# Optimization experiments

Hardware: AMD Instinct MI355X
Metric: run time of the kernel (lower is better)

The kernel has to match this reference:

```python
import jax, jax.numpy as jnp
import numpy as np

B, NQ, NK, D, H = 4, 1025, 1024, 1024, 16
C = D // H          # per-head channels = 64
DFF = 1024          # FFN hidden, hard-coded in source
LN_EPS = 1e-5


def setup_inputs() -> dict:
    key = jax.random.key(0)
    ks = jax.random.split(key, 12)
    s = 0.02
    return {
        "q": jax.random.normal(ks[0], (B, NQ, D), jnp.float32),
        "k": jax.random.normal(ks[1], (B, NK, D), jnp.float32),
        "v": jax.random.normal(ks[2], (B, NK, D), jnp.float32),
        "w_qk": jax.random.normal(ks[3], (D, D), jnp.float32) * s,
        "dummy": jax.random.normal(ks[4], (1, D), jnp.float32),
        "w1": jax.random.normal(ks[5], (C, C // 2), jnp.float32) * s,
        "b1": jnp.zeros((C // 2,), jnp.float32),
        "w2": jax.random.normal(ks[6], (C, C // 2), jnp.float32) * s,
        "b2": jnp.zeros((C // 2,), jnp.float32),
        "w3": jax.random.normal(ks[7], (2 * C, C), jnp.float32) * s,
        "b3": jnp.zeros((C,), jnp.float32),
        "fw1": jax.random.normal(ks[8], (C, DFF), jnp.float32) * s,
        "fb1": jnp.zeros((DFF,), jnp.float32),
        "fw2": jax.random.normal(ks[9], (DFF, C), jnp.float32) * s,
        "fb2": jnp.zeros((C,), jnp.float32),
        "ln_g": jnp.ones((C,), jnp.float32),
        "ln_b": jnp.zeros((C,), jnp.float32),
    }


def _split_heads(x):
    # 'b n (h c) -> (b h) n c'
    b, n, _ = x.shape
    return x.reshape(b, n, H, C).transpose(0, 2, 1, 3).reshape(b * H, n, C)


def _l2norm(x):
    n = jnp.linalg.norm(x, axis=-1, keepdims=True)
    return x / jnp.maximum(n, 1e-12)


def reference(q, k, v, w_qk, dummy, w1, b1, w2, b2, w3, b3,
              fw1, fb1, fw2, fb2, ln_g, ln_b):
    b, nq, d = q.shape
    residual = q
    qp = q @ w_qk
    kp = jnp.concatenate(
        [k @ w_qk, jnp.broadcast_to(dummy[None], (b, 1, d))], axis=1)
    vp = jnp.concatenate([v, jnp.zeros((b, 1, d), v.dtype)], axis=1)

    qh, kh, vh, rh = map(_split_heads, (qp, kp, vp, residual))

    # cosine-similarity attention, ReLU instead of softmax (dropout p=0)
    attn = jnp.einsum('bic,bjc->bij', _l2norm(qh), _l2norm(kh))
    attn = jax.nn.relu(attn)
    out = jnp.einsum('bij,bjc->bic', attn, vh)  # (b*h, nq, c)

    o1 = jax.nn.relu((out * rh) @ w1 + b1)
    o2 = jax.nn.relu((rh - out) @ w2 + b2)
    o = jnp.concatenate([o1, o2, rh], axis=-1) @ w3 + b3

    # FFN with residual + LayerNorm (dropouts are identity at p=0)
    t = o + rh
    t = t + (jax.nn.relu(t @ fw1 + fb1) @ fw2 + fb2)
    mu = jnp.mean(t, axis=-1, keepdims=True)
    var = jnp.mean(jnp.square(t - mu), axis=-1, keepdims=True)
    t = (t - mu) / jnp.sqrt(var + LN_EPS) * ln_g + ln_b

    t = t + vh  # requires nq == nk + 1

    # '(b h) n c -> b n (h c)'
    return t.reshape(b, H, nq, C).transpose(0, 2, 1, 3).reshape(b, nq, d)
```

## Files before the change

### kernel.cpp

```cpp
#include <hip/hip_runtime.h>
#include <hip/hip_bf16.h>

#define DEV __device__ __forceinline__

typedef __attribute__((ext_vector_type(4))) float  f32x4;
typedef __attribute__((ext_vector_type(8))) short  s16x8;
typedef __attribute__((ext_vector_type(8))) __bf16 bf16x8;

#define NQ   1025
#define BH   64
#define NPAD 1152
#define MT   65600
#define DFF  1024

DEV short f2bf(float f){
  unsigned u = __builtin_bit_cast(unsigned, f);
  u = u + 0x7fffu + ((u >> 16) & 1u);
  return (short)(u >> 16);
}
DEV float bf2f(short s){
  unsigned u = ((unsigned)(unsigned short)s) << 16;
  return __builtin_bit_cast(float, u);
}
DEV f32x4 zero4(){ f32x4 z; z[0]=0.f; z[1]=0.f; z[2]=0.f; z[3]=0.f; return z; }
DEV s16x8 zero8(){ s16x8 z; for(int e=0;e<8;e++) z[e]=0; return z; }

DEV f32x4 mfma16(s16x8 a, s16x8 b, f32x4 c){
  return __builtin_amdgcn_mfma_f32_16x16x32_bf16(
      __builtin_bit_cast(bf16x8, a), __builtin_bit_cast(bf16x8, b), c, 0, 0, 0);
}

DEV void gll16(const void* g, void* l){
  __builtin_amdgcn_global_load_lds((const __attribute__((address_space(1))) void*)g,
                                   (__attribute__((address_space(3))) void*)l, 16, 0, 0);
}

DEV s16x8 lds_frag(const char* base, int row, int k8){
  int byte = row*128 + k8*2; byte ^= (row & 7) << 4;
  return *(const s16x8*)(base + byte);
}
DEV void lds_write16(char* base, int row, int k8, s16x8 v){
  int byte = row*128 + k8*2; byte ^= (row & 7) << 4;
  *(s16x8*)(base + byte) = v;
}
DEV void lds_write2(char* base, int row, int col, short v){
  int byte = row*128 + col*2; byte ^= (row & 7) << 4;
  *(short*)(base + byte) = v;
}
DEV void lds_w16_256(char* base, int row, int col, s16x8 v){
  int byte = row*256 + col*2; byte ^= (row & 7) << 4;
  *(s16x8*)(base + byte) = v;
}
DEV s16x8 lds_r16_256(const char* base, int row, int col){
  int byte = row*256 + col*2; byte ^= (row & 7) << 4;
  return *(const s16x8*)(base + byte);
}
DEV void lds_w2_256(char* base, int row, int col, short v){
  int byte = row*256 + col*2; byte ^= (row & 7) << 4;
  *(short*)(base + byte) = v;
}
DEV void blob_w16(char* blob, int row, int k8, s16x8 v){
  int byte = row*128 + k8*2; byte ^= (row & 7) << 4;
  *(s16x8*)(blob + byte) = v;
}

__global__ __launch_bounds__(256)
void k_prep(const float* __restrict__ q, const float* __restrict__ kk,
            const float* __restrict__ v, const float* __restrict__ w_qk,
            const float* __restrict__ fw1, const float* __restrict__ fw2,
            char* __restrict__ ab, char* __restrict__ wb,
            char* __restrict__ vb, char* __restrict__ f1B, char* __restrict__ f2B){
  __shared__ float SMF[64*129];
  int bid = blockIdx.x;
  int tid = threadIdx.x;
  if (bid < 1152){
    int mt = bid>>4, kt = bid&15;
    int r = tid>>1, ks = (tid&1)*32;
    int pr = mt*128 + r;
    int part = pr >= 4608;
    int pp = part ? pr-4608 : pr;
    int b = pp/NPAD, i = pp%NPAD;
    const float* src = nullptr;
    if (!part && i < 1025) src = q  + ((long)(b*1025+i))*1024 + kt*64 + ks;
    if ( part && i < 1024) src = kk + ((long)(b*1024+i))*1024 + kt*64 + ks;
    char* blob = ab + ((long)(mt*16+kt))*16384;
    #pragma unroll
    for (int c8=0;c8<32;c8+=8){
      s16x8 vv = zero8();
      if (src){
        f32x4 f0 = *(const f32x4*)(src + c8);
        f32x4 f1 = *(const f32x4*)(src + c8 + 4);
        #pragma unroll
        for(int e=0;e<4;e++){ vv[e]=f2bf(f0[e]); vv[4+e]=f2bf(f1[e]); }
      }
      blob_w16(blob, r, ks+c8, vv);
    }
  } else if (bid < 1280){
    int loc = bid - 1152;
    int nt = loc>>4, kt = loc&15;
    float (*T)[129] = (float(*)[129])SMF;
    for (int idx=tid; idx<8192; idx+=256){
      int kr = idx>>7, nc = idx&127;
      T[kr][nc] = w_qk[(long)(kt*64+kr)*1024 + nt*128+nc];
    }
    __syncthreads();
    int r = tid>>1, ks=(tid&1)*32;
    char* blob = wb + ((long)(nt*16+kt))*16384;
    #pragma unroll
    for (int c8=0;c8<32;c8+=8){
      s16x8 vv;
      #pragma unroll
      for(int e=0;e<8;e++) vv[e] = f2bf(T[ks+c8+e][r]);
      blob_w16(blob, r, ks+c8, vv);
    }
  } else if (bid < 2304){
    int loc = bid - 1280;
    int jt = loc&15, bh = loc>>4;
    int b = bh>>4, h = bh&15;
    float (*T)[65] = (float(*)[65])SMF;
    for (int idx=tid; idx<4096; idx+=256){
      int jr = idx>>6, cc = idx&63;
      int j = jt*64+jr;
      T[jr][cc] = (j<1024)? v[((long)(b*1024+j))*1024 + h*64+cc] : 0.f;
    }
    __syncthreads();
    int r = tid>>2, js=(tid&3)*16;
    char* blob = vb + ((long)(bh*18+jt))*8192;
    #pragma unroll
    for (int c8=0;c8<16;c8+=8){
      s16x8 vv;
      #pragma unroll
      for(int e=0;e<8;e++) vv[e] = f2bf(T[js+c8+e][r]);
      blob_w16(blob, r, js+c8, vv);
    }
  } else {
    int loc = bid - 2304;
    int d = loc&15, which = loc>>4;
    float (*T)[65] = (float(*)[65])SMF;
    for (int idx=tid; idx<4096; idx+=256){
      int r = idx>>6, c = idx&63;
      T[r][c] = (which==0) ? fw1[(long)r*DFF + d*64 + c]
                           : fw2[(long)(d*64+r)*64 + c];
    }
    __syncthreads();
    char* blob = (which==0 ? f1B : f2B) + (long)d*8192;
    int rr = tid>>2, js = (tid&3)*16;
    #pragma unroll
    for (int c8=0;c8<16;c8+=8){
      s16x8 vv;
      #pragma unroll
      for(int e=0;e<8;e++) vv[e] = f2bf(T[js+c8+e][rr]);
      blob_w16(blob, rr, js+c8, vv);
    }
  }
}

__global__ __launch_bounds__(256,2)
void k_proj(const char* __restrict__ ab, const char* __restrict__ wb,
            char* __restrict__ qpB, char* __restrict__ kpB,
            float* __restrict__ qnorm, float* __restrict__ knorm){
  __shared__ char SM[32768];
  char* A = SM; char* Bm = SM+16384;
  int flat = blockIdx.x;
  int g = (flat&7)*72 + (flat>>3);
  int mt = g>>3, nt = g&7;
  int tid=threadIdx.x, lane=tid&63, wv=tid>>6, lr=lane&15, lg=lane>>4;
  f32x4 acc[4][4];
  for(int a=0;a<4;a++) for(int b=0;b<4;b++) acc[a][b]=zero4();
  int wm=(wv>>1)*64, wn=(wv&1)*64;
  for (int kt=0; kt<16; kt++){
    const char* asrc = ab + ((long)(mt*16+kt))*16384 + wv*4096 + lane*16;
    const char* bsrc = wb + ((long)(nt*16+kt))*16384 + wv*4096 + lane*16;
    char* adst = A + wv*4096;  char* bdst = Bm + wv*4096;
    #pragma unroll
    for (int t=0;t<4;t++){
      gll16(asrc + t*1024, adst + t*1024);
      gll16(bsrc + t*1024, bdst + t*1024);
    }
    __syncthreads();
    #pragma unroll
    for (int kc=0;kc<64;kc+=32){
      int lk = kc + (lg<<3);
      s16x8 af[4], bfr[4];
      #pragma unroll
      for(int i=0;i<4;i++) af[i]  = lds_frag(A,  wm + i*16 + lr, lk);
      #pragma unroll
      for(int i=0;i<4;i++) bfr[i] = lds_frag(Bm, wn + i*16 + lr, lk);
      #pragma unroll
      for(int mi=0;mi<4;mi++)
        #pragma unroll
        for(int ni=0;ni<4;ni++) acc[mi][ni] = mfma16(af[mi], bfr[ni], acc[mi][ni]);
    }
    __syncthreads();
  }
  int head = nt*2 + (wv&1);
  #pragma unroll
  for(int mi=0;mi<4;mi++)
  #pragma unroll
  for(int j=0;j<4;j++){
    float ss = 0.f;
    #pragma unroll
    for(int ni=0;ni<4;ni++){ float x=acc[mi][ni][j]; ss += x*x; }
    ss += __shfl_xor(ss,1); ss += __shfl_xor(ss,2);
    ss += __shfl_xor(ss,4); ss += __shfl_xor(ss,8);
    if (lr==0){
      int pr = mt*128 + wm + mi*16 + lg*4 + j;
      int part = pr>=4608; int pp = part? pr-4608:pr;
      int b = pp/NPAD, i = pp%NPAD;
      float scv = 1.f/fmaxf(sqrtf(ss), 1e-12f);
      (part? knorm : qnorm)[(b*16+head)*NPAD + i] = scv;
    }
  }
  #pragma unroll
  for(int mi=0;mi<4;mi++)
  #pragma unroll
  for(int ni=0;ni<4;ni++)
  #pragma unroll
  for(int j=0;j<4;j++)
    lds_w2_256(SM, wm+mi*16+lg*4+j, wn+ni*16+lr, f2bf(acc[mi][ni][j]));
  __syncthreads();
  {
    int r = tid>>1, half = tid&1;
    int pr = mt*128 + r;
    int part = pr>=4608; int pp = part? pr-4608:pr;
    int b = pp/NPAD, i = pp%NPAD;
    int h2 = nt*2 + half;
    char* dst = (part? kpB : qpB) + ((long)((b*16+h2)*18 + (i>>6)))*8192;
    int rr = i&63;
    #pragma unroll
    for (int c8=0;c8<64;c8+=8){
      s16x8 vv = lds_r16_256(SM, r, half*64 + c8);
      blob_w16(dst, rr, c8, vv);
    }
  }
}

__global__ __launch_bounds__(256,2)
void k_attn(const char* __restrict__ qpB, const char* __restrict__ kpB,
            const char* __restrict__ vtB,
            const float* __restrict__ qnorm, const float* __restrict__ knorm,
            short* __restrict__ att){
  __shared__ char SM[49152];
  char* Q = SM; char* KT = SM+16384; char* VT = KT+8192; char* P = VT+8192;
  int flat = blockIdx.x;
  int g = (flat&7)*72 + (flat>>3);
  int bh = g/9, it = g%9;
  int i0 = it*128;
  int tid=threadIdx.x, lane=tid&63, wv=tid>>6, lr=lane&15, lg=lane>>4;
  {
    const char* src = qpB + ((long)(bh*18 + it*2))*8192 + wv*4096 + lane*16;
    char* dst = Q + wv*4096;
    #pragma unroll
    for (int t=0;t<4;t++) gll16(src + t*1024, dst + t*1024);
  }
  float rq[2][4];
  #pragma unroll
  for(int mi=0;mi<2;mi++)
  #pragma unroll
  for(int j=0;j<4;j++)
    rq[mi][j] = qnorm[bh*NPAD + i0 + wv*32+mi*16+lg*4+j];
  f32x4 oacc[2][4];
  for(int a=0;a<2;a++) for(int b=0;b<4;b++) oacc[a][b]=zero4();
  for (int jt=0; jt<16; ++jt){
    {
      const char* ks = kpB + ((long)(bh*18+jt))*8192 + wv*2048 + lane*16;
      const char* vs = vtB + ((long)(bh*18+jt))*8192 + wv*2048 + lane*16;
      gll16(ks,      KT + wv*2048);
      gll16(ks+1024, KT + wv*2048 + 1024);
      gll16(vs,      VT + wv*2048);
      gll16(vs+1024, VT + wv*2048 + 1024);
    }
    float rk[4];
    #pragma unroll
    for(int ni=0;ni<4;ni++) rk[ni] = knorm[bh*NPAD + jt*64 + ni*16+lr];
    __syncthreads();
    f32x4 sc[2][4];
    for(int a=0;a<2;a++) for(int b=0;b<4;b++) sc[a][b]=zero4();
    #pragma unroll
    for(int kc=0;kc<64;kc+=32){
      int lk = kc + (lg<<3);
      s16x8 af[2], bfr[4];
      #pragma unroll
      for(int i=0;i<2;i++) af[i]=lds_frag(Q, wv*32 + i*16 + lr, lk);
      #pragma unroll
      for(int i=0;i<4;i++) bfr[i]=lds_frag(KT, i*16 + lr, lk);
      #pragma unroll
      for(int mi=0;mi<2;mi++)
        #pragma unroll
        for(int ni=0;ni<4;ni++) sc[mi][ni]=mfma16(af[mi],bfr[ni],sc[mi][ni]);
    }
    #pragma unroll
    for(int mi=0;mi<2;mi++)
    #pragma unroll
    for(int ni=0;ni<4;ni++)
    #pragma unroll
    for(int j=0;j<4;j++){
      float x = sc[mi][ni][j] * rq[mi][j] * rk[ni];
      x = x>0.f?x:0.f;
      lds_write2(P, wv*32 + mi*16 + lg*4 + j, ni*16 + lr, f2bf(x));
    }
    __syncthreads();
    #pragma unroll
    for(int kc=0;kc<64;kc+=32){
      int lk = kc + (lg<<3);
      s16x8 pf[2], vf[4];
      #pragma unroll
      for(int i=0;i<2;i++) pf[i]=lds_frag(P, wv*32 + i*16 + lr, lk);
      #pragma unroll
      for(int i=0;i<4;i++) vf[i]=lds_frag(VT, i*16 + lr, lk);
      #pragma unroll
      for(int mi=0;mi<2;mi++)
        #pragma unroll
        for(int ni=0;ni<4;ni++) oacc[mi][ni]=mfma16(pf[mi],vf[ni],oacc[mi][ni]);
    }
    __syncthreads();
  }
  char* OS = SM+16384;
  #pragma unroll
  for(int mi=0;mi<2;mi++)
  #pragma unroll
  for(int ni=0;ni<4;ni++)
  #pragma unroll
  for(int j=0;j<4;j++)
    lds_write2(OS, wv*32+mi*16+lg*4+j, ni*16+lr, f2bf(oacc[mi][ni][j]));
  __syncthreads();
  {
    int r = tid>>1, half = tid&1;
    int i = i0 + r;
    if (i < 1025){
      short* dst = att + ((long)bh*1025 + i)*64 + half*32;
      #pragma unroll
      for (int u=0; u<32; u+=8){
        s16x8 vv = lds_frag(OS, r, half*32 + u);
        *(s16x8*)(dst + u) = vv;
      }
    }
  }
}

__global__ __launch_bounds__(512,4)
void k_tailpre(const short* __restrict__ att, const float* __restrict__ q,
    const float* __restrict__ w1, const float* __restrict__ b1,
    const float* __restrict__ w2, const float* __restrict__ b2,
    const float* __restrict__ w3, const float* __restrict__ b3,
    float* __restrict__ tf){
  __shared__ char SM[73728];
  char* R1 = SM;
  char* R2 = SM + 16384;
  char* R3 = SM + 32768;
  char* WA = SM + 49152;
  char* WB = SM + 53248;
  char* W3 = SM + 57344;
  long m0 = (long)blockIdx.x*128;
  int tid=threadIdx.x, lane=tid&63, wv=tid>>6, lr=lane&15, lg=lane>>4;
  int wr0 = wv*16;
  for (int idx=tid; idx<2048; idx+=512){
    int n=idx>>6, c=idx&63;
    lds_write2(WA, n, c, f2bf(w1[c*32+n]));
    lds_write2(WB, n, c, f2bf(w2[c*32+n]));
  }
  for (int idx=tid; idx<8192; idx+=512){
    int n=idx>>7, kx=idx&127;
    lds_w2_256(W3, n, kx, f2bf(w3[kx*64+n]));
  }
  {
    int r = tid>>2, ks=(tid&3)*16;
    long m = m0 + r;
    if (m < MT){
      int bh=(int)(m/1025); int i=(int)(m-(long)bh*1025); int b=bh>>4, h=bh&15;
      const short* asrc = att + m*64 + ks;
      const float* qsrc = q + ((long)b*1025+i)*1024 + h*64 + ks;
      #pragma unroll
      for (int c8=0;c8<16;c8+=8){
        s16x8 av = *(const s16x8*)(asrc + c8);
        f32x4 q0 = *(const f32x4*)(qsrc + c8);
        f32x4 q1 = *(const f32x4*)(qsrc + c8 + 4);
        s16x8 x1v,x2v,rhv;
        #pragma unroll
        for(int e=0;e<4;e++){
          float o0=bf2f(av[e]),   r0=q0[e];
          float o1=bf2f(av[4+e]), r1=q1[e];
          x1v[e]=f2bf(o0*r0);   x1v[4+e]=f2bf(o1*r1);
          x2v[e]=f2bf(r0-o0);   x2v[4+e]=f2bf(r1-o1);
          rhv[e]=f2bf(r0);      rhv[4+e]=f2bf(r1);
        }
        lds_write16(R1, r, ks+c8, x1v);
        lds_write16(R2, r, ks+c8, x2v);
        lds_write16(R3, r, ks+c8, rhv);
      }
    } else {
      s16x8 z = zero8();
      #pragma unroll
      for (int c8=0;c8<16;c8+=8){
        lds_write16(R1, r, ks+c8, z);
        lds_write16(R2, r, ks+c8, z);
        lds_write16(R3, r, ks+c8, z);
      }
    }
  }
  __syncthreads();
  f32x4 a1[4];
  #pragma unroll
  for(int ni=0;ni<4;ni++) a1[ni]=zero4();
  #pragma unroll
  for (int kc=0;kc<64;kc+=32){
    int lk = kc + (lg<<3);
    s16x8 af1 = lds_frag(R1, wr0+lr, lk);
    s16x8 af2 = lds_frag(R2, wr0+lr, lk);
    s16x8 bw1[2], bw2[2];
    #pragma unroll
    for(int i=0;i<2;i++){
      bw1[i]=lds_frag(WA, i*16+lr, lk);
      bw2[i]=lds_frag(WB, i*16+lr, lk);
    }
    #pragma unroll
    for(int ni=0;ni<2;ni++){
      a1[ni]   = mfma16(af1, bw1[ni], a1[ni]);
      a1[2+ni] = mfma16(af2, bw2[ni], a1[2+ni]);
    }
  }
  float bias12[4];
  #pragma unroll
  for(int ni=0;ni<4;ni++){ int cc=ni*16+lr; bias12[ni] = (cc<32)? b1[cc] : b2[cc-32]; }
  #pragma unroll
  for(int ni=0;ni<4;ni++)
  #pragma unroll
  for(int j=0;j<4;j++){
    float x = a1[ni][j] + bias12[ni];
    x = x>0.f?x:0.f;
    lds_write2(R1, wr0+lg*4+j, ni*16+lr, f2bf(x));
  }
  f32x4 a2[4];
  #pragma unroll
  for(int ni=0;ni<4;ni++) a2[ni]=zero4();
  #pragma unroll
  for (int kc=0;kc<64;kc+=32){
    int lk = kc + (lg<<3);
    s16x8 ao = lds_frag(R1, wr0+lr, lk);
    s16x8 ar = lds_frag(R3, wr0+lr, lk);
    s16x8 bo[4], br[4];
    #pragma unroll
    for(int i=0;i<4;i++){
      bo[i]=lds_r16_256(W3, i*16+lr, lk);
      br[i]=lds_r16_256(W3, i*16+lr, 64+lk);
    }
    #pragma unroll
    for(int ni=0;ni<4;ni++){
      a2[ni]=mfma16(ao, bo[ni], a2[ni]);
      a2[ni]=mfma16(ar, br[ni], a2[ni]);
    }
  }
  float b3v[4];
  #pragma unroll
  for(int ni=0;ni<4;ni++) b3v[ni] = b3[ni*16+lr];
  #pragma unroll
  for(int j=0;j<4;j++){
    long m = m0 + wr0 + lg*4 + j;
    if (m < MT){
      int bh=(int)(m/1025); int i=(int)(m-(long)bh*1025); int b=bh>>4, h=bh&15;
      const float* qsrc = q + ((long)b*1025+i)*1024 + h*64;
      #pragma unroll
      for(int ni=0;ni<4;ni++){
        int cc = ni*16+lr;
        tf[m*64+cc] = a2[ni][j] + b3v[ni] + qsrc[cc];
      }
    }
  }
}

__global__ __launch_bounds__(256,3)
void k_ffn(const float* __restrict__ tf,
      const char* __restrict__ f1B, const char* __restrict__ f2B,
      const float* __restrict__ fb1, const float* __restrict__ fb2,
      const float* __restrict__ ln_g, const float* __restrict__ ln_b,
      const float* __restrict__ v, float* __restrict__ out){
  __shared__ char SM[49152];
  char* T  = SM;
  char* U  = SM + 16384;
  char* W1 = SM + 32768;
  char* W2 = SM + 40960;
  long m0 = (long)blockIdx.x*128;
  int tid=threadIdx.x, lane=tid&63, wv=tid>>6, lr=lane&15, lg=lane>>4;
  {
    int r=tid>>1, ks=(tid&1)*32; long m=m0+r;
    #pragma unroll
    for(int c8=0;c8<32;c8+=8){
      s16x8 vv = zero8();
      if (m<MT){
        f32x4 f0 = *(const f32x4*)(tf + m*64 + ks + c8);
        f32x4 f1 = *(const f32x4*)(tf + m*64 + ks + c8 + 4);
        #pragma unroll
        for(int e=0;e<4;e++){ vv[e]=f2bf(f0[e]); vv[4+e]=f2bf(f1[e]); }
      }
      lds_write16(T, r, ks+c8, vv);
    }
  }
  f32x4 acc2[2][4];
  for(int a=0;a<2;a++) for(int b=0;b<4;b++) acc2[a][b]=zero4();
  for (int d=0; d<16; ++d){
    {
      const char* s1 = f1B + (long)d*8192 + wv*2048 + lane*16;
      const char* s2 = f2B + (long)d*8192 + wv*2048 + lane*16;
      gll16(s1,        W1 + wv*2048);
      gll16(s1 + 1024, W1 + wv*2048 + 1024);
      gll16(s2,        W2 + wv*2048);
      gll16(s2 + 1024, W2 + wv*2048 + 1024);
    }
    __syncthreads();
    f32x4 sc[2][4];
    for(int a=0;a<2;a++) for(int b=0;b<4;b++) sc[a][b]=zero4();
    #pragma unroll
    for(int kc=0;kc<64;kc+=32){
      int lk = kc + (lg<<3);
      s16x8 af[2], bfr[4];
      #pragma unroll
      for(int i=0;i<2;i++) af[i]=lds_frag(T, wv*32+i*16+lr, lk);
      #pragma unroll
      for(int i=0;i<4;i++) bfr[i]=lds_frag(W1, i*16+lr, lk);
      #pragma unroll
      for(int mi=0;mi<2;mi++)
        #pragma unroll
        for(int ni=0;ni<4;ni++) sc[mi][ni]=mfma16(af[mi],bfr[ni],sc[mi][ni]);
    }
    #pragma unroll
    for(int mi=0;mi<2;mi++)
    #pragma unroll
    for(int ni=0;ni<4;ni++)
    #pragma unroll
    for(int j=0;j<4;j++){
      int uc = ni*16+lr;
      float x = sc[mi][ni][j] + fb1[d*64+uc];
      x = x>0.f?x:0.f;
      lds_write2(U, wv*32+mi*16+lg*4+j, uc, f2bf(x));
    }
    #pragma unroll
    for(int kc=0;kc<64;kc+=32){
      int lk = kc + (lg<<3);
      s16x8 uf[2], wf[4];
      #pragma unroll
      for(int i=0;i<2;i++) uf[i]=lds_frag(U, wv*32+i*16+lr, lk);
      #pragma unroll
      for(int i=0;i<4;i++) wf[i]=lds_frag(W2, i*16+lr, lk);
      #pragma unroll
      for(int mi=0;mi<2;mi++)
        #pragma unroll
        for(int ni=0;ni<4;ni++) acc2[mi][ni]=mfma16(uf[mi],wf[ni],acc2[mi][ni]);
    }
    __syncthreads();
  }
  #pragma unroll
  for(int mi=0;mi<2;mi++){
    float xv[4][4];
    long mbase = m0 + wv*32 + mi*16 + lg*4;
    #pragma unroll
    for(int ni=0;ni<4;ni++)
    #pragma unroll
    for(int j=0;j<4;j++){
      long m = mbase + j;
      int c = ni*16+lr;
      float t = (m<MT)? tf[m*64+c] : 0.f;
      xv[ni][j] = acc2[mi][ni][j] + fb2[c] + t;
    }
    #pragma unroll
    for(int j=0;j<4;j++){
      float s = xv[0][j]+xv[1][j]+xv[2][j]+xv[3][j];
      #pragma unroll
      for(int mm=1;mm<16;mm<<=1) s += __shfl_xor(s, mm);
      float mu = s*(1.f/64.f);
      float vs = 0.f;
      #pragma unroll
      for(int ni=0;ni<4;ni++){ float d2=xv[ni][j]-mu; vs += d2*d2; }
      #pragma unroll
      for(int mm=1;mm<16;mm<<=1) vs += __shfl_xor(vs, mm);
      float inv = rsqrtf(vs*(1.f/64.f) + 1e-5f);
      long m = mbase + j;
      if (m < MT){
        int bh = (int)(m/1025); int i = (int)(m - (long)bh*1025);
        int b = bh>>4, h = bh&15;
        #pragma unroll
        for(int ni=0;ni<4;ni++){
          int c = ni*16+lr;
          float y = (xv[ni][j]-mu)*inv*ln_g[c] + ln_b[c];
          float vh = (i<1024)? v[((long)b*1024 + i)*1024 + h*64 + c] : 0.f;
          out[((long)b*1025 + i)*1024 + h*64 + c] = y + vh;
        }
      }
    }
  }
}

extern "C" void kernel_launch(void* const* d_in, const int* in_sizes, int n_in,
                              void* d_out, int out_size, void* d_ws, size_t ws_size,
                              hipStream_t stream) {
  const float* q    = (const float*)d_in[0];
  const float* k    = (const float*)d_in[1];
  const float* v    = (const float*)d_in[2];
  const float* w_qk = (const float*)d_in[3];
  const float* w1   = (const float*)d_in[5];
  const float* b1   = (const float*)d_in[6];
  const float* w2   = (const float*)d_in[7];
  const float* b2   = (const float*)d_in[8];
  const float* w3   = (const float*)d_in[9];
  const float* b3   = (const float*)d_in[10];
  const float* fw1  = (const float*)d_in[11];
  const float* fb1  = (const float*)d_in[12];
  const float* fw2  = (const float*)d_in[13];
  const float* fb2  = (const float*)d_in[14];
  const float* ln_g = (const float*)d_in[15];
  const float* ln_b = (const float*)d_in[16];
  float* out = (float*)d_out;

  char* ws = (char*)d_ws;
  const size_t OFF_A   = 0;
  const size_t SZ_A    = 25190400;
  const size_t OFF_WB  = OFF_A + SZ_A;
  const size_t OFF_F1B = OFF_WB  + (size_t)8*16*16384;
  const size_t OFF_F2B = OFF_F1B + (size_t)16*8192;
  const size_t OFF_VT  = OFF_F2B + (size_t)16*8192;
  const size_t OFF_QP  = OFF_VT  + (size_t)64*18*8192;
  const size_t OFF_KP  = OFF_QP  + (size_t)64*18*8192;
  const size_t OFF_QN  = OFF_KP  + (size_t)64*18*8192;
  const size_t OFF_KN  = OFF_QN  + (size_t)BH*NPAD*4;
  const size_t NEEDED  = OFF_KN  + (size_t)BH*NPAD*4;
  if (ws_size < NEEDED) return;

  char*  ab   = ws + OFF_A;
  short* att  = (short*)(ws + OFF_A);
  float* tf   = (float*)(ws + OFF_A + 8396800);
  char*  wb   = ws + OFF_WB;
  char*  f1B  = ws + OFF_F1B;
  char*  f2B  = ws + OFF_F2B;
  char*  vtB  = ws + OFF_VT;
  char*  qpB  = ws + OFF_QP;
  char*  kpB  = ws + OFF_KP;
  float* qnorm= (float*)(ws + OFF_QN);
  float* knorm= (float*)(ws + OFF_KN);

  k_prep<<<2336, 256, 0, stream>>>(q, k, v, w_qk, fw1, fw2, ab, wb, vtB, f1B, f2B);
  k_proj<<<576, 256, 0, stream>>>(ab, wb, qpB, kpB, qnorm, knorm);
  k_attn<<<576, 256, 0, stream>>>(qpB, kpB, vtB, qnorm, knorm, att);
  k_tailpre<<<513, 512, 0, stream>>>(att, q, w1, b1, w2, b2, w3, b3, tf);
  k_ffn<<<513, 256, 0, stream>>>(tf, f1B, f2B, fb1, fb2, ln_g, ln_b, v, out);
}
```

Before: 179.6 us.

## Handle lone trailing query row separately and skip padded tiles in projection

Query length is 1025, so the last 128-row attention tile held only one real row. That tile is replaced by 64 small blocks, one per batch-head, which compute the final query row with scalar dot products against K and a direct fp32 reduction over V. The projection grid is also cut from 576 to 544 blocks by remapping M-tile indices so that all-padding tiles are skipped. The intent is to remove wasted MFMA work on padding. The cost is a slower scalar path for the tail row, whose strided V reads may lengthen the critical path.

Result: no change. 181.0 us (+0.7%).

```diff
diff --git a/kernel.cpp b/kernel.cpp
--- a/kernel.cpp
+++ b/kernel.cpp
@@ -162,8 +162,9 @@
   __shared__ char SM[32768];
   char* A = SM; char* Bm = SM+16384;
   int flat = blockIdx.x;
-  int g = (flat&7)*72 + (flat>>3);
-  int mt = g>>3, nt = g&7;
+  int g = (flat&7)*68 + (flat>>3);
+  int mtIdx = g>>3, nt = g&7;
+  int mt = (mtIdx < 44) ? mtIdx : (mtIdx + 1 + (mtIdx-44)/8);
   int tid=threadIdx.x, lane=tid&63, wv=tid>>6, lr=lane&15, lg=lane>>4;
   f32x4 acc[4][4];
   for(int a=0;a<4;a++) for(int b=0;b<4;b++) acc[a][b]=zero4();
@@ -239,14 +240,57 @@
 void k_attn(const char* __restrict__ qpB, const char* __restrict__ kpB,
             const char* __restrict__ vtB,
             const float* __restrict__ qnorm, const float* __restrict__ knorm,
-            short* __restrict__ att){
+            const float* __restrict__ v, short* __restrict__ att){
   __shared__ char SM[49152];
+  int flat = blockIdx.x;
+  int tid=threadIdx.x, lane=tid&63, wv=tid>>6, lr=lane&15, lg=lane>>4;
+  if (flat >= 512){
+    int bh = flat - 512;
+    int b = bh>>4, h = bh&15;
+    float* XS = (float*)SM;
+    float* RS = (float*)(SM + 4096);
+    const short* qrow = (const short*)(qpB + ((long)(bh*18+16))*8192);
+    float rqv = qnorm[bh*NPAD + 1024];
+    float qv[64];
+    #pragma unroll
+    for (int c8=0;c8<64;c8+=8){
+      s16x8 qq = *(const s16x8*)(qrow + c8);
+      #pragma unroll
+      for(int e=0;e<8;e++) qv[c8+e] = bf2f(qq[e]);
+    }
+    for (int p=0;p<4;p++){
+      int j = tid + 256*p;
+      const char* kb = kpB + ((long)(bh*18+(j>>6)))*8192;
+      int r = j&63;
+      float S = 0.f;
+      #pragma unroll
+      for (int c8=0;c8<64;c8+=8){
+        s16x8 kv = lds_frag(kb, r, c8);
+        #pragma unroll
+        for(int e=0;e<8;e++) S += qv[c8+e]*bf2f(kv[e]);
+      }
+      float x = S * rqv * knorm[bh*NPAD + j];
+      XS[j] = x>0.f ? x : 0.f;
+    }
+    __syncthreads();
+    float acc = 0.f;
+    const float* vb = v + (long)b*1024*1024 + h*64 + lane;
+    for (int p=0;p<256;p++){
+      int j = wv*256 + p;
+      acc += XS[j] * vb[(long)j*1024];
+    }
+    RS[wv*64 + lane] = acc;
+    __syncthreads();
+    if (tid < 64){
+      float tot = RS[tid] + RS[64+tid] + RS[128+tid] + RS[192+tid];
+      att[((long)bh*1025 + 1024)*64 + tid] = f2bf(tot);
+    }
+    return;
+  }
   char* Q = SM; char* KT = SM+16384; char* VT = KT+8192; char* P = VT+8192;
-  int flat = blockIdx.x;
-  int g = (flat&7)*72 + (flat>>3);
-  int bh = g/9, it = g%9;
+  int g = (flat&7)*64 + (flat>>3);
+  int bh = g>>3, it = g&7;
   int i0 = it*128;
-  int tid=threadIdx.x, lane=tid&63, wv=tid>>6, lr=lane&15, lg=lane>>4;
   {
     const char* src = qpB + ((long)(bh*18 + it*2))*8192 + wv*4096 + lane*16;
     char* dst = Q + wv*4096;
@@ -327,13 +371,11 @@
   {
     int r = tid>>1, half = tid&1;
     int i = i0 + r;
-    if (i < 1025){
-      short* dst = att + ((long)bh*1025 + i)*64 + half*32;
-      #pragma unroll
-      for (int u=0; u<32; u+=8){
-        s16x8 vv = lds_frag(OS, r, half*32 + u);
-        *(s16x8*)(dst + u) = vv;
-      }
+    short* dst = att + ((long)bh*1025 + i)*64 + half*32;
+    #pragma unroll
+    for (int u=0; u<32; u+=8){
+      s16x8 vv = lds_frag(OS, r, half*32 + u);
+      *(s16x8*)(dst + u) = vv;
     }
   }
 }
@@ -637,8 +679,8 @@
   float* knorm= (float*)(ws + OFF_KN);
 
   k_prep<<<2336, 256, 0, stream>>>(q, k, v, w_qk, fw1, fw2, ab, wb, vtB, f1B, f2B);
-  k_proj<<<576, 256, 0, stream>>>(ab, wb, qpB, kpB, qnorm, knorm);
-  k_attn<<<576, 256, 0, stream>>>(qpB, kpB, vtB, qnorm, knorm, att);
+  k_proj<<<544, 256, 0, stream>>>(ab, wb, qpB, kpB, qnorm, knorm);
+  k_attn<<<576, 256, 0, stream>>>(qpB, kpB, vtB, qnorm, knorm, v, att);
   k_tailpre<<<513, 512, 0, stream>>>(att, q, w1, b1, w2, b2, w3, b3, tf);
   k_ffn<<<513, 256, 0, stream>>>(tf, f1B, f2B, fb1, fb2, ln_g, ln_b, v, out);
 }
```
